# Performance work log

Hardware: AMD Instinct MI355X
Metric: run time of the kernel (lower is better)

## Reference

```python
import jax, jax.numpy as jnp
import numpy as np

N_NODES = 131072          # total nodes across all expressions
NODES_PER_EXPR = 64       # nodes per expression (left or right side)
NUM_SEG = N_NODES // NODES_PER_EXPR   # 2048 segments = 1024 equations x 2 sides
VOCAB = 320
D_MODEL = 128
NUM_LAYERS = 4


def setup_inputs() -> dict:
    key = jax.random.key(0)
    ks = jax.random.split(key, 8)
    # combined-vocab index per node (leaf->token id, internal->function id + offset)
    node_idx = jax.random.randint(ks[0], (N_NODES,), 0, VOCAB)
    # 4 incoming edges per node: left child, right child, parent, self.
    # index N_NODES is the padding node (zero features).
    nb = jax.random.randint(ks[1], (N_NODES, 3), 0, N_NODES + 1)
    self_col = jnp.arange(N_NODES)[:, None]
    neighbors = jnp.concatenate([nb, self_col], axis=1)  # [N, 4]
    # contiguous expression segments (matches batched DGL graph layout)
    seg_ids = jnp.arange(N_NODES) // NODES_PER_EXPR
    emb = jax.random.normal(ks[2], (VOCAB, D_MODEL), dtype=jnp.float32) * 0.02
    W0 = jax.random.normal(ks[3], (NUM_LAYERS, 4 * D_MODEL, D_MODEL), dtype=jnp.float32) * (1.0 / np.sqrt(4 * D_MODEL))
    b0 = jnp.zeros((NUM_LAYERS, D_MODEL), dtype=jnp.float32)
    W1 = jax.random.normal(ks[4], (NUM_LAYERS, D_MODEL, D_MODEL), dtype=jnp.float32) * (1.0 / np.sqrt(D_MODEL))
    b1 = jnp.zeros((NUM_LAYERS, D_MODEL), dtype=jnp.float32)
    out_bias = jnp.zeros((1,), dtype=jnp.float32)
    return {"node_idx": node_idx, "neighbors": neighbors, "seg_ids": seg_ids,
            "emb": emb, "W0": W0, "b0": b0, "W1": W1, "b1": b1, "out_bias": out_bias}


def reference(node_idx, neighbors, seg_ids, emb, W0, b0, W1, b1, out_bias):
    N, d = node_idx.shape[0], emb.shape[1]
    feats = emb[node_idx]                                   # [N, d] embedding lookup
    num_layers = W0.shape[0]
    for l in range(num_layers):
        # padding node (id N) always contributes zero features
        f_pad = jnp.concatenate([feats, jnp.zeros((1, d), feats.dtype)], axis=0)
        gathered = f_pad[neighbors].reshape(N, 4 * d)       # [N, 4d] mailbox gather+flatten
        h = jax.nn.relu(gathered @ W0[l] + b0[l])           # FunctionModule layer 1
        feats = h @ W1[l] + b1[l]                           # FunctionModule layer 2
    # per-expression mean feature (graph readout)
    sums = jax.ops.segment_sum(feats, seg_ids, num_segments=NUM_SEG)      # [2B, d]
    cnts = jax.ops.segment_sum(jnp.ones((N,), feats.dtype), seg_ids, num_segments=NUM_SEG)
    means = sums / cnts[:, None]
    means = means.reshape(-1, 2, d)                         # [B, 2, d] (left, right)
    logits = jnp.einsum('bd,bd->b', means[:, 0], means[:, 1]) + out_bias[0]
    return logits
```

## Files before the change

### kernel.cpp

```cpp
#include <hip/hip_runtime.h>

#define N_NODES 131072
#define D 128
#define NLAYERS 4
#define AS_STRIDE 136

typedef _Float16 f16;
typedef _Float16 f16x8 __attribute__((ext_vector_type(8)));
typedef _Float16 f16x4 __attribute__((ext_vector_type(4)));
typedef float f32x4 __attribute__((ext_vector_type(4)));

__global__ __launch_bounds__(256) void prep_weights(
    const float* __restrict__ W0, const float* __restrict__ W1,
    f16* __restrict__ W0t, f16* __restrict__ W1t)
{
    __shared__ float T[64][65];
    int b = blockIdx.x;
    const float* src; f16* dst; int K, tk, tn;
    if (b < 64) {
        int l = b >> 4; tk = (b >> 1) & 7; tn = b & 1;
        src = W0 + (size_t)l * 512 * 128; dst = W0t + (size_t)l * 128 * 512; K = 512;
    } else {
        int bb = b - 64; int l = bb >> 2; tk = (bb >> 1) & 1; tn = bb & 1;
        src = W1 + (size_t)l * 128 * 128; dst = W1t + (size_t)l * 128 * 128; K = 128;
    }
    const int tid = threadIdx.x;
#pragma unroll
    for (int i = 0; i < 16; ++i) {
        int u = tid + 256 * i;
        int kk = u >> 6, nn = u & 63;
        T[kk][nn] = src[(size_t)(tk * 64 + kk) * 128 + tn * 64 + nn];
    }
    __syncthreads();
#pragma unroll
    for (int i = 0; i < 16; ++i) {
        int u = tid + 256 * i;
        int nn = u >> 6, kk = u & 63;
        dst[(size_t)(tn * 64 + nn) * K + tk * 64 + kk] = (f16)T[kk][nn];
    }
}

__global__ __launch_bounds__(256) void embed_f16(
    const int* __restrict__ node_idx, const float* __restrict__ emb,
    f16* __restrict__ fa, f16* __restrict__ fb)
{
    const int tid = threadIdx.x;
    if (blockIdx.x == 16384) {
        if (tid < 32) {
            f16x8 z = {0, 0, 0, 0, 0, 0, 0, 0};
            f16* base = (tid >> 4) ? fb : fa;
            *(f16x8*)&base[(size_t)N_NODES * D + (tid & 15) * 8] = z;
        }
        return;
    }
    int i = blockIdx.x * 256 + tid;
    int v = i >> 5, c = i & 31;
    int tok = node_idx[v];
    float4 x = ((const float4*)emb)[(size_t)tok * 32 + c];
    f16x4 y = { (f16)x.x, (f16)x.y, (f16)x.z, (f16)x.w };
    *(f16x4*)&fa[(size_t)v * D + c * 4] = y;
}

__global__ __launch_bounds__(256, 2) void layer_fused(
    const f16* __restrict__ fin, f16* __restrict__ fout,
    const int* __restrict__ neighbors,
    const f16* __restrict__ W0t, const float* __restrict__ b0,
    const f16* __restrict__ W1t, const float* __restrict__ b1)
{
    __shared__ f16 As[128][AS_STRIDE];
    __shared__ f16 Bs[128][AS_STRIDE];
    __shared__ int nbr_s[512];

    const int tid  = threadIdx.x;
    const int bm   = blockIdx.x * 128;
    const int lane = tid & 63;
    const int wave = tid >> 6;
    const int wr = wave >> 1, wc = wave & 1;
    const int quad = lane >> 4, lm = lane & 15;
    const int seg = tid & 15, r0 = tid >> 4;

    nbr_s[tid]       = neighbors[bm * 4 + tid];
    nbr_s[tid + 256] = neighbors[bm * 4 + 256 + tid];

    float bb0[4], bb1[4];
#pragma unroll
    for (int c = 0; c < 4; ++c) {
        bb0[c] = b0[wc * 64 + c * 16 + lm];
        bb1[c] = b1[wc * 64 + c * 16 + lm];
    }

    f16x8 ra[8], rb[8];
    __syncthreads();

#pragma unroll
    for (int i = 0; i < 8; ++i) {
        int row = r0 + 16 * i;
        int nbr = nbr_s[row * 4 + 0];
        ra[i] = *(const f16x8*)&fin[(size_t)nbr * D + seg * 8];
        rb[i] = *(const f16x8*)&W0t[(size_t)row * 512 + seg * 8];
    }
#pragma unroll
    for (int i = 0; i < 8; ++i) {
        int row = r0 + 16 * i;
        *(f16x8*)&As[row][seg * 8] = ra[i];
        *(f16x8*)&Bs[row][seg * 8] = rb[i];
    }
    __syncthreads();

    f32x4 acc1[4][4];
#pragma unroll
    for (int r = 0; r < 4; ++r)
#pragma unroll
        for (int c = 0; c < 4; ++c) acc1[r][c] = (f32x4){0.f, 0.f, 0.f, 0.f};

    for (int e = 0; e < 4; ++e) {
        if (e < 3) {
#pragma unroll
            for (int i = 0; i < 8; ++i) {
                int row = r0 + 16 * i;
                int nbr = nbr_s[row * 4 + e + 1];
                ra[i] = *(const f16x8*)&fin[(size_t)nbr * D + seg * 8];
                rb[i] = *(const f16x8*)&W0t[(size_t)row * 512 + (e + 1) * 128 + seg * 8];
            }
        } else {
#pragma unroll
            for (int i = 0; i < 8; ++i) {
                int row = r0 + 16 * i;
                rb[i] = *(const f16x8*)&W1t[(size_t)row * 128 + seg * 8];
            }
        }
#pragma unroll
        for (int t = 0; t < 4; ++t) {
            const int k0 = t * 32 + quad * 8;
            f16x8 af[4], bf[4];
#pragma unroll
            for (int r = 0; r < 4; ++r)
                af[r] = *(const f16x8*)&As[wr * 64 + r * 16 + lm][k0];
#pragma unroll
            for (int c = 0; c < 4; ++c)
                bf[c] = *(const f16x8*)&Bs[wc * 64 + c * 16 + lm][k0];
#pragma unroll
            for (int r = 0; r < 4; ++r)
#pragma unroll
                for (int c = 0; c < 4; ++c)
                    acc1[r][c] = __builtin_amdgcn_mfma_f32_16x16x32_f16(
                        af[r], bf[c], acc1[r][c], 0, 0, 0);
        }
        __syncthreads();
        if (e < 3) {
#pragma unroll
            for (int i = 0; i < 8; ++i) {
                int row = r0 + 16 * i;
                *(f16x8*)&As[row][seg * 8] = ra[i];
                *(f16x8*)&Bs[row][seg * 8] = rb[i];
            }
            __syncthreads();
        }
    }

    unsigned int hpk[4][4][2];
#pragma unroll
    for (int c = 0; c < 4; ++c) {
#pragma unroll
        for (int r = 0; r < 4; ++r) {
#pragma unroll
            for (int p = 0; p < 2; ++p) {
                float v0 = fmaxf(acc1[r][c][2 * p]     + bb0[c], 0.f);
                float v1 = fmaxf(acc1[r][c][2 * p + 1] + bb0[c], 0.f);
                unsigned short u0 = __builtin_bit_cast(unsigned short, (f16)v0);
                unsigned short u1 = __builtin_bit_cast(unsigned short, (f16)v1);
                hpk[r][c][p] = ((unsigned)u1 << 16) | u0;
            }
        }
    }

#pragma unroll
    for (int r = 0; r < 4; ++r)
#pragma unroll
        for (int c = 0; c < 4; ++c) {
            int gcol = wc * 64 + c * 16 + lm;
#pragma unroll
            for (int reg = 0; reg < 4; ++reg) {
                int grow = wr * 64 + r * 16 + quad * 4 + reg;
                unsigned pk = hpk[r][c][reg >> 1];
                unsigned short bits = (reg & 1) ? (unsigned short)(pk >> 16)
                                                : (unsigned short)(pk & 0xffff);
                As[grow][gcol] = __builtin_bit_cast(f16, bits);
            }
        }
#pragma unroll
    for (int i = 0; i < 8; ++i) {
        int row = r0 + 16 * i;
        *(f16x8*)&Bs[row][seg * 8] = rb[i];
    }
    __syncthreads();

    f32x4 acc2[4][4];
#pragma unroll
    for (int r = 0; r < 4; ++r)
#pragma unroll
        for (int c = 0; c < 4; ++c) acc2[r][c] = (f32x4){0.f, 0.f, 0.f, 0.f};

#pragma unroll
    for (int t = 0; t < 4; ++t) {
        const int k0 = t * 32 + quad * 8;
        f16x8 af[4], bf[4];
#pragma unroll
        for (int r = 0; r < 4; ++r)
            af[r] = *(const f16x8*)&As[wr * 64 + r * 16 + lm][k0];
#pragma unroll
        for (int c = 0; c < 4; ++c)
            bf[c] = *(const f16x8*)&Bs[wc * 64 + c * 16 + lm][k0];
#pragma unroll
        for (int r = 0; r < 4; ++r)
#pragma unroll
            for (int c = 0; c < 4; ++c)
                acc2[r][c] = __builtin_amdgcn_mfma_f32_16x16x32_f16(
                    af[r], bf[c], acc2[r][c], 0, 0, 0);
    }
    __syncthreads();

#pragma unroll
    for (int r = 0; r < 4; ++r)
#pragma unroll
        for (int c = 0; c < 4; ++c) {
            int gcol = wc * 64 + c * 16 + lm;
#pragma unroll
            for (int reg = 0; reg < 4; ++reg) {
                int grow = wr * 64 + r * 16 + quad * 4 + reg;
                As[grow][gcol] = (f16)(acc2[r][c][reg] + bb1[c]);
            }
        }
    __syncthreads();
#pragma unroll
    for (int i = 0; i < 8; ++i) {
        int row = r0 + 16 * i;
        *(f16x8*)&fout[(size_t)(bm + row) * D + seg * 8] =
            *(const f16x8*)&As[row][seg * 8];
    }
}

__global__ __launch_bounds__(256) void readout_f16(
    const f16* __restrict__ feats, const float* __restrict__ out_bias,
    float* __restrict__ logits)
{
    __shared__ float ms[2][128];
    const int b   = blockIdx.x;
    const int tid = threadIdx.x;
    const int side = tid >> 7, d = tid & 127;

    const f16* base = feats + ((size_t)b * 128 + side * 64) * D + d;
    float s = 0.f;
#pragma unroll 8
    for (int n = 0; n < 64; ++n) s += (float)base[(size_t)n * D];
    ms[side][d] = s * (1.0f / 64.0f);
    __syncthreads();

    if (tid < 64) {
        float v = ms[0][tid] * ms[1][tid] + ms[0][tid + 64] * ms[1][tid + 64];
#pragma unroll
        for (int off = 32; off; off >>= 1) v += __shfl_down(v, off);
        if (tid == 0) logits[b] = v + out_bias[0];
    }
}

extern "C" void kernel_launch(void* const* d_in, const int* in_sizes, int n_in,
                              void* d_out, int out_size, void* d_ws, size_t ws_size,
                              hipStream_t stream) {
    const int*   node_idx  = (const int*)d_in[0];
    const int*   neighbors = (const int*)d_in[1];
    const float* emb       = (const float*)d_in[3];
    const float* W0        = (const float*)d_in[4];
    const float* b0        = (const float*)d_in[5];
    const float* W1        = (const float*)d_in[6];
    const float* b1        = (const float*)d_in[7];
    const float* out_bias  = (const float*)d_in[8];
    float*       logits    = (float*)d_out;

    const size_t NP1 = (size_t)N_NODES + 1;
    f16* feats_a = (f16*)d_ws;
    f16* feats_b = feats_a + NP1 * D;
    f16* W0t     = feats_b + NP1 * D;
    f16* W1t     = W0t + (size_t)NLAYERS * 512 * 128;

    prep_weights<<<80, 256, 0, stream>>>(W0, W1, W0t, W1t);
    embed_f16<<<16385, 256, 0, stream>>>(node_idx, emb, feats_a, feats_b);

    f16* fin = feats_a; f16* fout = feats_b;
    for (int l = 0; l < NLAYERS; ++l) {
        layer_fused<<<N_NODES / 128, 256, 0, stream>>>(
            fin, fout, neighbors,
            W0t + (size_t)l * 512 * 128, b0 + (size_t)l * 128,
            W1t + (size_t)l * 128 * 128, b1 + (size_t)l * 128);
        f16* t = fin; fin = fout; fout = t;
    }
    readout_f16<<<N_NODES / 128, 256, 0, stream>>>(feats_a, out_bias, logits);
}
```

Measured before the change: 244.8 us.

## Fuse embedding lookup into first layer and deepen gather prefetch

Removes the separate embedding kernel: the first layer gathers token ids and fp32 embedding rows directly for each neighbor, converts them to f16 and writes them to shared memory, so the full embedded feature array is never written out and reread. The padding-row zeroing moves into the weight-prep kernel. The mid-layer kernels now prefetch two neighbor tiles ahead and load the next weight slice after each barrier, giving more gather latency hiding. The cost is higher register pressure from the extra buffers, plus the fp32 embedding reads and the indirect node_idx lookups inside the first GEMM kernel. Ping-pong buffers and the readout input are adjusted to match.

```diff
diff --git a/kernel.cpp b/kernel.cpp
--- a/kernel.cpp
+++ b/kernel.cpp
@@ -7,15 +7,24 @@
 
 typedef _Float16 f16;
 typedef _Float16 f16x8 __attribute__((ext_vector_type(8)));
-typedef _Float16 f16x4 __attribute__((ext_vector_type(4)));
 typedef float f32x4 __attribute__((ext_vector_type(4)));
 
 __global__ __launch_bounds__(256) void prep_weights(
     const float* __restrict__ W0, const float* __restrict__ W1,
-    f16* __restrict__ W0t, f16* __restrict__ W1t)
+    f16* __restrict__ W0t, f16* __restrict__ W1t,
+    f16* __restrict__ fa, f16* __restrict__ fb)
 {
     __shared__ float T[64][65];
     int b = blockIdx.x;
+    const int tid = threadIdx.x;
+    if (b == 80) {
+        if (tid < 32) {
+            f16x8 z = {0, 0, 0, 0, 0, 0, 0, 0};
+            f16* base = (tid >> 4) ? fb : fa;
+            *(f16x8*)&base[(size_t)N_NODES * D + (tid & 15) * 8] = z;
+        }
+        return;
+    }
     const float* src; f16* dst; int K, tk, tn;
     if (b < 64) {
         int l = b >> 4; tk = (b >> 1) & 7; tn = b & 1;
@@ -24,7 +33,6 @@
         int bb = b - 64; int l = bb >> 2; tk = (bb >> 1) & 1; tn = bb & 1;
         src = W1 + (size_t)l * 128 * 128; dst = W1t + (size_t)l * 128 * 128; K = 128;
     }
-    const int tid = threadIdx.x;
 #pragma unroll
     for (int i = 0; i < 16; ++i) {
         int u = tid + 256 * i;
@@ -40,28 +48,205 @@
     }
 }
 
-__global__ __launch_bounds__(256) void embed_f16(
+#define COMPUTE_STAGE(ACC)                                                   \
+    _Pragma("unroll")                                                        \
+    for (int t = 0; t < 4; ++t) {                                            \
+        const int k0 = t * 32 + quad * 8;                                    \
+        f16x8 af[4], bf[4];                                                  \
+        _Pragma("unroll")                                                    \
+        for (int r = 0; r < 4; ++r)                                          \
+            af[r] = *(const f16x8*)&As[wr * 64 + r * 16 + lm][k0];           \
+        _Pragma("unroll")                                                    \
+        for (int c = 0; c < 4; ++c)                                          \
+            bf[c] = *(const f16x8*)&Bs[wc * 64 + c * 16 + lm][k0];           \
+        _Pragma("unroll")                                                    \
+        for (int r = 0; r < 4; ++r)                                          \
+            _Pragma("unroll")                                                \
+            for (int c = 0; c < 4; ++c)                                      \
+                ACC[r][c] = __builtin_amdgcn_mfma_f32_16x16x32_f16(          \
+                    af[r], bf[c], ACC[r][c], 0, 0, 0);                       \
+    }
+
+#define TAIL_PHASE2_EPILOGUE()                                               \
+           \
+    _Pragma("unroll")                                                        \
+    for (int r = 0; r < 4; ++r)                                              \
+        _Pragma("unroll")                                                    \
+        for (int c = 0; c < 4; ++c) {                                        \
+            int gcol = wc * 64 + c * 16 + lm;                                \
+            _Pragma("unroll")                                                \
+            for (int reg = 0; reg < 4; ++reg) {                              \
+                int grow = wr * 64 + r * 16 + quad * 4 + reg;                \
+                unsigned pk = hpk[r][c][reg >> 1];                           \
+                unsigned short bits = (reg & 1) ? (unsigned short)(pk >> 16) \
+                                                : (unsigned short)(pk & 0xffff); \
+                As[grow][gcol] = __builtin_bit_cast(f16, bits);              \
+            }                                                                \
+        }                                                                    \
+    _Pragma("unroll")                                                        \
+    for (int i = 0; i < 8; ++i) {                                            \
+        int row = r0 + 16 * i;                                               \
+        *(f16x8*)&Bs[row][seg * 8] = rb[i];                                  \
+    }                                                                        \
+    __syncthreads();                                                         \
+    f32x4 acc2[4][4];                                                        \
+    _Pragma("unroll")                                                        \
+    for (int r = 0; r < 4; ++r)                                              \
+        _Pragma("unroll")                                                    \
+        for (int c = 0; c < 4; ++c) acc2[r][c] = (f32x4){0.f, 0.f, 0.f, 0.f};\
+    COMPUTE_STAGE(acc2)                                                      \
+    __syncthreads();                                                         \
+    _Pragma("unroll")                                                        \
+    for (int r = 0; r < 4; ++r)                                              \
+        _Pragma("unroll")                                                    \
+        for (int c = 0; c < 4; ++c) {                                        \
+            int gcol = wc * 64 + c * 16 + lm;                                \
+            _Pragma("unroll")                                                \
+            for (int reg = 0; reg < 4; ++reg) {                              \
+                int grow = wr * 64 + r * 16 + quad * 4 + reg;                \
+                As[grow][gcol] = (f16)(acc2[r][c][reg] + bb1[c]);            \
+            }                                                                \
+        }                                                                    \
+    __syncthreads();                                                         \
+    _Pragma("unroll")                                                        \
+    for (int i = 0; i < 8; ++i) {                                            \
+        int row = r0 + 16 * i;                                               \
+        *(f16x8*)&fout[(size_t)(bm + row) * D + seg * 8] =                   \
+            *(const f16x8*)&As[row][seg * 8];                                \
+    }
+
+#define PACK_H()                                                             \
+    unsigned int hpk[4][4][2];                                               \
+    _Pragma("unroll")                                                        \
+    for (int c = 0; c < 4; ++c) {                                            \
+        _Pragma("unroll")                                                    \
+        for (int r = 0; r < 4; ++r) {                                        \
+            _Pragma("unroll")                                                \
+            for (int p = 0; p < 2; ++p) {                                    \
+                float v0 = fmaxf(acc1[r][c][2 * p]     + bb0[c], 0.f);       \
+                float v1 = fmaxf(acc1[r][c][2 * p + 1] + bb0[c], 0.f);       \
+                unsigned short u0 = __builtin_bit_cast(unsigned short, (f16)v0); \
+                unsigned short u1 = __builtin_bit_cast(unsigned short, (f16)v1); \
+                hpk[r][c][p] = ((unsigned)u1 << 16) | u0;                    \
+            }                                                                \
+        }                                                                    \
+    }
+
+__global__ __launch_bounds__(256, 2) void layer_emb(
     const int* __restrict__ node_idx, const float* __restrict__ emb,
-    f16* __restrict__ fa, f16* __restrict__ fb)
+    f16* __restrict__ fout, const int* __restrict__ neighbors,
+    const f16* __restrict__ W0t, const float* __restrict__ b0,
+    const f16* __restrict__ W1t, const float* __restrict__ b1)
 {
-    const int tid = threadIdx.x;
-    if (blockIdx.x == 16384) {
-        if (tid < 32) {
-            f16x8 z = {0, 0, 0, 0, 0, 0, 0, 0};
-            f16* base = (tid >> 4) ? fb : fa;
-            *(f16x8*)&base[(size_t)N_NODES * D + (tid & 15) * 8] = z;
-        }
-        return;
-    }
-    int i = blockIdx.x * 256 + tid;
-    int v = i >> 5, c = i & 31;
-    int tok = node_idx[v];
-    float4 x = ((const float4*)emb)[(size_t)tok * 32 + c];
-    f16x4 y = { (f16)x.x, (f16)x.y, (f16)x.z, (f16)x.w };
-    *(f16x4*)&fa[(size_t)v * D + c * 4] = y;
+    __shared__ f16 As[128][AS_STRIDE];
+    __shared__ f16 Bs[128][AS_STRIDE];
+    __shared__ int nbr_s[512];
+
+    const int tid  = threadIdx.x;
+    const int bm   = blockIdx.x * 128;
+    const int lane = tid & 63;
+    const int wave = tid >> 6;
+    const int wr = wave >> 1, wc = wave & 1;
+    const int quad = lane >> 4, lm = lane & 15;
+    const int seg = tid & 15, r0 = tid >> 4;
+
+    nbr_s[tid]       = neighbors[bm * 4 + tid];
+    nbr_s[tid + 256] = neighbors[bm * 4 + 256 + tid];
+
+    float bb0[4], bb1[4];
+#pragma unroll
+    for (int c = 0; c < 4; ++c) {
+        bb0[c] = b0[wc * 64 + c * 16 + lm];
+        bb1[c] = b1[wc * 64 + c * 16 + lm];
+    }
+
+    float4 rg[8][2];
+    f16x8 rb[8];
+    __syncthreads();
+
+#pragma unroll
+    for (int i = 0; i < 8; ++i) {
+        int row = r0 + 16 * i;
+        int nbr = nbr_s[row * 4 + 0];
+        float4 z = make_float4(0.f, 0.f, 0.f, 0.f);
+        rg[i][0] = z; rg[i][1] = z;
+        if (nbr < N_NODES) {
+            int tok = node_idx[nbr];
+            const float4* p = (const float4*)emb + (size_t)tok * 32 + seg * 2;
+            rg[i][0] = p[0]; rg[i][1] = p[1];
+        }
+    }
+#pragma unroll
+    for (int i = 0; i < 8; ++i) {
+        int row = r0 + 16 * i;
+        rb[i] = *(const f16x8*)&W0t[(size_t)row * 512 + seg * 8];
+    }
+#pragma unroll
+    for (int i = 0; i < 8; ++i) {
+        int row = r0 + 16 * i;
+        float4 a = rg[i][0], bq = rg[i][1];
+        f16x8 v = { (f16)a.x, (f16)a.y, (f16)a.z, (f16)a.w,
+                    (f16)bq.x, (f16)bq.y, (f16)bq.z, (f16)bq.w };
+        *(f16x8*)&As[row][seg * 8] = v;
+        *(f16x8*)&Bs[row][seg * 8] = rb[i];
+    }
+    __syncthreads();
+#pragma unroll
+    for (int i = 0; i < 8; ++i) {
+        int row = r0 + 16 * i;
+        rb[i] = *(const f16x8*)&W0t[(size_t)row * 512 + 128 + seg * 8];
+    }
+
+    f32x4 acc1[4][4];
+#pragma unroll
+    for (int r = 0; r < 4; ++r)
+#pragma unroll
+        for (int c = 0; c < 4; ++c) acc1[r][c] = (f32x4){0.f, 0.f, 0.f, 0.f};
+
+#pragma unroll
+    for (int e = 0; e < 4; ++e) {
+        if (e < 3) {
+#pragma unroll
+            for (int i = 0; i < 8; ++i) {
+                int row = r0 + 16 * i;
+                int nbr = nbr_s[row * 4 + e + 1];
+                float4 z = make_float4(0.f, 0.f, 0.f, 0.f);
+                rg[i][0] = z; rg[i][1] = z;
+                if (nbr < N_NODES) {
+                    int tok = node_idx[nbr];
+                    const float4* p = (const float4*)emb + (size_t)tok * 32 + seg * 2;
+                    rg[i][0] = p[0]; rg[i][1] = p[1];
+                }
+            }
+        }
+        COMPUTE_STAGE(acc1)
+        __syncthreads();
+        if (e < 3) {
+#pragma unroll
+            for (int i = 0; i < 8; ++i) {
+                int row = r0 + 16 * i;
+                float4 a = rg[i][0], bq = rg[i][1];
+                f16x8 v = { (f16)a.x, (f16)a.y, (f16)a.z, (f16)a.w,
+                            (f16)bq.x, (f16)bq.y, (f16)bq.z, (f16)bq.w };
+                *(f16x8*)&As[row][seg * 8] = v;
+                *(f16x8*)&Bs[row][seg * 8] = rb[i];
+            }
+            __syncthreads();
+#pragma unroll
+            for (int i = 0; i < 8; ++i) {
+                int row = r0 + 16 * i;
+                rb[i] = (e < 2)
+                    ? *(const f16x8*)&W0t[(size_t)row * 512 + (e + 2) * 128 + seg * 8]
+                    : *(const f16x8*)&W1t[(size_t)row * 128 + seg * 8];
+            }
+        }
+    }
+
+    PACK_H()
+    TAIL_PHASE2_EPILOGUE()
 }
 
-__global__ __launch_bounds__(256, 2) void layer_fused(
+__global__ __launch_bounds__(256, 2) void layer_mid(
     const f16* __restrict__ fin, f16* __restrict__ fout,
     const int* __restrict__ neighbors,
     const f16* __restrict__ W0t, const float* __restrict__ b0,
@@ -89,23 +274,36 @@
         bb1[c] = b1[wc * 64 + c * 16 + lm];
     }
 
-    f16x8 ra[8], rb[8];
-    __syncthreads();
-
-#pragma unroll
-    for (int i = 0; i < 8; ++i) {
-        int row = r0 + 16 * i;
-        int nbr = nbr_s[row * 4 + 0];
-        ra[i] = *(const f16x8*)&fin[(size_t)nbr * D + seg * 8];
+    f16x8 ra0[8], ra1[8], rb[8];
+    __syncthreads();
+
+#pragma unroll
+    for (int i = 0; i < 8; ++i) {
+        int row = r0 + 16 * i;
+        ra0[i] = *(const f16x8*)&fin[(size_t)nbr_s[row * 4 + 0] * D + seg * 8];
+    }
+#pragma unroll
+    for (int i = 0; i < 8; ++i) {
+        int row = r0 + 16 * i;
+        ra1[i] = *(const f16x8*)&fin[(size_t)nbr_s[row * 4 + 1] * D + seg * 8];
+    }
+#pragma unroll
+    for (int i = 0; i < 8; ++i) {
+        int row = r0 + 16 * i;
         rb[i] = *(const f16x8*)&W0t[(size_t)row * 512 + seg * 8];
     }
 #pragma unroll
     for (int i = 0; i < 8; ++i) {
         int row = r0 + 16 * i;
-        *(f16x8*)&As[row][seg * 8] = ra[i];
+        *(f16x8*)&As[row][seg * 8] = ra0[i];
         *(f16x8*)&Bs[row][seg * 8] = rb[i];
     }
     __syncthreads();
+#pragma unroll
+    for (int i = 0; i < 8; ++i) {
+        int row = r0 + 16 * i;
+        rb[i] = *(const f16x8*)&W0t[(size_t)row * 512 + 128 + seg * 8];
+    }
 
     f32x4 acc1[4][4];
 #pragma unroll
@@ -113,131 +311,43 @@
 #pragma unroll
         for (int c = 0; c < 4; ++c) acc1[r][c] = (f32x4){0.f, 0.f, 0.f, 0.f};
 
+#pragma unroll
     for (int e = 0; e < 4; ++e) {
-        if (e < 3) {
-#pragma unroll
-            for (int i = 0; i < 8; ++i) {
-                int row = r0 + 16 * i;
-                int nbr = nbr_s[row * 4 + e + 1];
-                ra[i] = *(const f16x8*)&fin[(size_t)nbr * D + seg * 8];
-                rb[i] = *(const f16x8*)&W0t[(size_t)row * 512 + (e + 1) * 128 + seg * 8];
-            }
-        } else {
-#pragma unroll
-            for (int i = 0; i < 8; ++i) {
-                int row = r0 + 16 * i;
-                rb[i] = *(const f16x8*)&W1t[(size_t)row * 128 + seg * 8];
-            }
-        }
-#pragma unroll
-        for (int t = 0; t < 4; ++t) {
-            const int k0 = t * 32 + quad * 8;
-            f16x8 af[4], bf[4];
-#pragma unroll
-            for (int r = 0; r < 4; ++r)
-                af[r] = *(const f16x8*)&As[wr * 64 + r * 16 + lm][k0];
-#pragma unroll
-            for (int c = 0; c < 4; ++c)
-                bf[c] = *(const f16x8*)&Bs[wc * 64 + c * 16 + lm][k0];
-#pragma unroll
-            for (int r = 0; r < 4; ++r)
-#pragma unroll
-                for (int c = 0; c < 4; ++c)
-                    acc1[r][c] = __builtin_amdgcn_mfma_f32_16x16x32_f16(
-                        af[r], bf[c], acc1[r][c], 0, 0, 0);
-        }
+        if (e == 0) {
+#pragma unroll
+            for (int i = 0; i < 8; ++i) {
+                int row = r0 + 16 * i;
+                ra0[i] = *(const f16x8*)&fin[(size_t)nbr_s[row * 4 + 2] * D + seg * 8];
+            }
+        } else if (e == 1) {
+#pragma unroll
+            for (int i = 0; i < 8; ++i) {
+                int row = r0 + 16 * i;
+                ra1[i] = *(const f16x8*)&fin[(size_t)nbr_s[row * 4 + 3] * D + seg * 8];
+            }
+        }
+        COMPUTE_STAGE(acc1)
         __syncthreads();
         if (e < 3) {
 #pragma unroll
             for (int i = 0; i < 8; ++i) {
                 int row = r0 + 16 * i;
-                *(f16x8*)&As[row][seg * 8] = ra[i];
+                *(f16x8*)&As[row][seg * 8] = (e & 1) ? ra0[i] : ra1[i];
                 *(f16x8*)&Bs[row][seg * 8] = rb[i];
             }
             __syncthreads();
-        }
-    }
-
-    unsigned int hpk[4][4][2];
-#pragma unroll
-    for (int c = 0; c < 4; ++c) {
-#pragma unroll
-        for (int r = 0; r < 4; ++r) {
-#pragma unroll
-            for (int p = 0; p < 2; ++p) {
-                float v0 = fmaxf(acc1[r][c][2 * p]     + bb0[c], 0.f);
-                float v1 = fmaxf(acc1[r][c][2 * p + 1] + bb0[c], 0.f);
-                unsigned short u0 = __builtin_bit_cast(unsigned short, (f16)v0);
-                unsigned short u1 = __builtin_bit_cast(unsigned short, (f16)v1);
-                hpk[r][c][p] = ((unsigned)u1 << 16) | u0;
-            }
-        }
-    }
-
-#pragma unroll
-    for (int r = 0; r < 4; ++r)
-#pragma unroll
-        for (int c = 0; c < 4; ++c) {
-            int gcol = wc * 64 + c * 16 + lm;
-#pragma unroll
-            for (int reg = 0; reg < 4; ++reg) {
-                int grow = wr * 64 + r * 16 + quad * 4 + reg;
-                unsigned pk = hpk[r][c][reg >> 1];
-                unsigned short bits = (reg & 1) ? (unsigned short)(pk >> 16)
-                                                : (unsigned short)(pk & 0xffff);
-                As[grow][gcol] = __builtin_bit_cast(f16, bits);
-            }
-        }
-#pragma unroll
-    for (int i = 0; i < 8; ++i) {
-        int row = r0 + 16 * i;
-        *(f16x8*)&Bs[row][seg * 8] = rb[i];
-    }
-    __syncthreads();
-
-    f32x4 acc2[4][4];
-#pragma unroll
-    for (int r = 0; r < 4; ++r)
-#pragma unroll
-        for (int c = 0; c < 4; ++c) acc2[r][c] = (f32x4){0.f, 0.f, 0.f, 0.f};
-
-#pragma unroll
-    for (int t = 0; t < 4; ++t) {
-        const int k0 = t * 32 + quad * 8;
-        f16x8 af[4], bf[4];
-#pragma unroll
-        for (int r = 0; r < 4; ++r)
-            af[r] = *(const f16x8*)&As[wr * 64 + r * 16 + lm][k0];
-#pragma unroll
-        for (int c = 0; c < 4; ++c)
-            bf[c] = *(const f16x8*)&Bs[wc * 64 + c * 16 + lm][k0];
-#pragma unroll
-        for (int r = 0; r < 4; ++r)
-#pragma unroll
-            for (int c = 0; c < 4; ++c)
-                acc2[r][c] = __builtin_amdgcn_mfma_f32_16x16x32_f16(
-                    af[r], bf[c], acc2[r][c], 0, 0, 0);
-    }
-    __syncthreads();
-
-#pragma unroll
-    for (int r = 0; r < 4; ++r)
-#pragma unroll
-        for (int c = 0; c < 4; ++c) {
-            int gcol = wc * 64 + c * 16 + lm;
-#pragma unroll
-            for (int reg = 0; reg < 4; ++reg) {
-                int grow = wr * 64 + r * 16 + quad * 4 + reg;
-                As[grow][gcol] = (f16)(acc2[r][c][reg] + bb1[c]);
-            }
-        }
-    __syncthreads();
-#pragma unroll
-    for (int i = 0; i < 8; ++i) {
-        int row = r0 + 16 * i;
-        *(f16x8*)&fout[(size_t)(bm + row) * D + seg * 8] =
-            *(const f16x8*)&As[row][seg * 8];
-    }
+#pragma unroll
+            for (int i = 0; i < 8; ++i) {
+                int row = r0 + 16 * i;
+                rb[i] = (e < 2)
+                    ? *(const f16x8*)&W0t[(size_t)row * 512 + (e + 2) * 128 + seg * 8]
+                    : *(const f16x8*)&W1t[(size_t)row * 128 + seg * 8];
+            }
+        }
+    }
+
+    PACK_H()
+    TAIL_PHASE2_EPILOGUE()
 }
 
 __global__ __launch_bounds__(256) void readout_f16(
@@ -283,16 +393,18 @@
     f16* W0t     = feats_b + NP1 * D;
     f16* W1t     = W0t + (size_t)NLAYERS * 512 * 128;
 
-    prep_weights<<<80, 256, 0, stream>>>(W0, W1, W0t, W1t);
-    embed_f16<<<16385, 256, 0, stream>>>(node_idx, emb, feats_a, feats_b);
+    prep_weights<<<81, 256, 0, stream>>>(W0, W1, W0t, W1t, feats_a, feats_b);
+
+    layer_emb<<<N_NODES / 128, 256, 0, stream>>>(
+        node_idx, emb, feats_a, neighbors, W0t, b0, W1t, b1);
 
     f16* fin = feats_a; f16* fout = feats_b;
-    for (int l = 0; l < NLAYERS; ++l) {
-        layer_fused<<<N_NODES / 128, 256, 0, stream>>>(
+    for (int l = 1; l < NLAYERS; ++l) {
+        layer_mid<<<N_NODES / 128, 256, 0, stream>>>(
             fin, fout, neighbors,
             W0t + (size_t)l * 512 * 128, b0 + (size_t)l * 128,
             W1t + (size_t)l * 128 * 128, b1 + (size_t)l * 128);
         f16* t = fin; fin = fout; fout = t;
     }
-    readout_f16<<<N_NODES / 128, 256, 0, stream>>>(feats_a, out_bias, logits);
+    readout_f16<<<N_NODES / 128, 256, 0, stream>>>(feats_b, out_bias, logits);
 }
```

Measured after the change: 238.1 us. -2.8%, faster.
